# Kernel optimization log

Hardware: AMD Instinct MI355X
Metric: run time of the kernel (lower is better)

## Reference

```python
import jax, jax.numpy as jnp
from jax import lax
import numpy as np

B, N = 2, 1024  # batch of NxN linear-system matrices
DN = ('NCHW', 'OIHW', 'NCHW')


def _conv(x, w, b, pad):
    # cross-correlation, same convention as torch/spconv
    return lax.conv_general_dilated(x, w, (1, 1), pad, dimension_numbers=DN) + b[None, :, None, None]


def _spread_mask(m, pad):
    # regular sparse conv: output site active iff any input site in 2x2 window is active
    ones = jnp.ones((1, 1, 2, 2), dtype=m.dtype)
    return (lax.conv_general_dilated(m, ones, (1, 1), pad, dimension_numbers=DN) > 0).astype(m.dtype)


def _prelu(x, a):
    return jnp.where(x >= 0, x, a * x)


def setup_inputs() -> dict:
    key = jax.random.key(0)
    ks = jax.random.split(key, 10)
    mask = jax.random.randint(ks[0], (B, N, N), 0, 2, dtype=jnp.int32)
    x = jax.random.normal(ks[1], (B, 1, N, N), dtype=jnp.float32)

    def w(k, o, i, kh, kw):
        return jax.random.normal(k, (o, i, kh, kw), dtype=jnp.float32) / np.sqrt(i * kh * kw)

    def bias(k, o):
        return 0.01 * jax.random.normal(k, (o,), dtype=jnp.float32)

    return {
        'x': x, 'mask': mask,
        'w1': w(ks[2], 8, 1, 1, 1), 'b1': bias(ks[6], 8), 'a1': jnp.float32(0.25),
        'w2': w(ks[3], 16, 8, 2, 2), 'b2': bias(ks[7], 16), 'a2': jnp.float32(0.25),
        'w3': w(ks[4], 8, 16, 2, 2), 'b3': bias(ks[8], 8), 'a3': jnp.float32(0.25),
        'w4': w(ks[5], 1, 8, 1, 1), 'b4': bias(ks[9], 1),
    }


def reference(x, mask, w1, b1, a1, w2, b2, a2, w3, b3, a3, w4, b4):
    m = (mask > 0).astype(jnp.float32)[:, None]          # [B,1,N,N] active-site mask
    h = x * m                                            # sparse input: zeros at inactive sites
    # layer 1: 1x1 conv + PReLU (mask unchanged)
    h = _conv(h, w1, b1, ((0, 0), (0, 0))) * m
    h = _prelu(h, a1)
    # layer 2: 2x2 conv, padding (1,0) -> [B,16,N+1,N-1]
    p2 = ((1, 1), (0, 0))
    m2 = _spread_mask(m, p2)
    h = _conv(h, w2, b2, p2) * m2
    h = _prelu(h, a2)
    # layer 3: 2x2 conv, padding (0,1) -> [B,8,N,N]
    p3 = ((0, 0), (1, 1))
    m3 = _spread_mask(m2, p3)
    h = _conv(h, w3, b3, p3) * m3
    h = _prelu(h, a3)
    # layer 4: 1x1 conv (mask unchanged)
    h = _conv(h, w4, b4, ((0, 0), (0, 0))) * m3          # [B,1,N,N]
    # triangular masking on sparse indices (row=indices[:,1], col=indices[:,2])
    row = jnp.arange(N)[:, None]
    col = jnp.arange(N)[None, :]
    h = jnp.where((row >= col)[None, None], h, jnp.float32(0))
    diag_active = (row == col)[None, None] & (m3 > 0)
    h = jnp.where(diag_active, jax.nn.softplus(h), h)
    return h
```

## Files before the change

### kernel.cpp

```cpp
#include <hip/hip_runtime.h>
#include <hip/hip_bf16.h>
#include <math.h>

#define N 1024
#define TB 16

typedef __attribute__((ext_vector_type(8))) short short8;
typedef __attribute__((ext_vector_type(4))) short short4v;
typedef __attribute__((ext_vector_type(4))) float f32x4;

__device__ __forceinline__ float prelu(float v, float a) {
    return fmaxf(v, a * v);
}

__device__ __forceinline__ short f2bf(float f) {
    return (short)__bfloat16_as_ushort(__float2bfloat16(f));
}

__global__ __launch_bounds__(256, 8) void precond_mfma(
    const float* __restrict__ xg, const int* __restrict__ maskg,
    const float* __restrict__ w1, const float* __restrict__ b1, const float* __restrict__ a1p,
    const float* __restrict__ w2, const float* __restrict__ b2, const float* __restrict__ a2p,
    const float* __restrict__ w3, const float* __restrict__ b3, const float* __restrict__ a3p,
    const float* __restrict__ w4, const float* __restrict__ b4p,
    float* __restrict__ out)
{
    const int tid = threadIdx.x;
    const int bz  = blockIdx.z;
    const int t   = blockIdx.x;

    int by = (int)((sqrtf(8.0f * (float)t + 1.0f) - 1.0f) * 0.5f);
    by += ((by + 1) * (by + 2) / 2 <= t);
    by -= (by * (by + 1) / 2 > t);
    const int bx = t - by * (by + 1) / 2;
    const int ty0 = by * TB, tx0 = bx * TB;
    const bool diag = (bx == by);

    const int lane = tid & 63, wid = tid >> 6;
    const int c16 = lane & 15, g = lane >> 4;

    const float w2r0 = w2[tid];
    const float w2r1 = w2[tid + 256];
    const float w3r0 = w3[tid];
    const float w3r1 = w3[tid + 256];

    const int pA0 = tid;
    const int pA1 = tid + 256;
    const bool s1valid = (pA1 < 324);
    const bool s1wave  = ((tid - lane) + 256 < 324);
    const int dyA0 = pA0 / 18, dxA0 = pA0 - dyA0 * 18;
    const int dyA1 = pA1 / 18, dxA1 = pA1 - dyA1 * 18;

    int gy0 = ty0 - 1 + dyA0, gx0 = tx0 - 1 + dxA0;
    const bool in0 = (unsigned)gy0 < N && (unsigned)gx0 < N;
    size_t i0 = in0 ? (((size_t)bz * N + gy0) * N + gx0) : 0;
    const int   mr0 = maskg[i0];
    const float xr0 = xg[i0];

    int mr1 = 0; float xr1 = 0.f; bool in1 = false;
    if (s1wave) {
        int gy1 = ty0 - 1 + dyA1, gx1 = tx0 - 1 + dxA1;
        in1 = s1valid && (unsigned)gy1 < N && (unsigned)gx1 < N;
        size_t i1 = in1 ? (((size_t)bz * N + gy1) * N + gx1) : 0;
        mr1 = maskg[i1];
        xr1 = xg[i1];
    }

    if (by < 63 && tid < 64) {
        int zy = bx * TB + (tid >> 2), zx = (by + 1) * TB + (tid & 3) * 4;
        *(float4*)&out[((size_t)bz * N + zy) * N + zx] = make_float4(0.f, 0.f, 0.f, 0.f);
    }

    __shared__ __align__(16) short sW2[512];
    __shared__ __align__(16) short sW3h[512];
    __shared__ __align__(16) short h1s[324 * 8];
    __shared__ __align__(16) short h2lo[4][85 * 8];
    __shared__ __align__(16) short h2hi[4][85 * 8];
    __shared__ __align__(16) unsigned RM1[12];

    const float a1 = a1p[0], a2 = a2p[0], a3 = a3p[0];
    const float b4 = b4p[0];
    const bool leftEdge  = (tx0 == 0);
    const bool rightEdge = (tx0 == N - TB);

    {
        int s0 = tid, s1 = tid + 256;
        sW2[(s0 & ~31) | ((s0 & 3) << 3) | ((s0 >> 2) & 7)] = f2bf(w2r0);
        sW2[(s1 & ~31) | ((s1 & 3) << 3) | ((s1 >> 2) & 7)] = f2bf(w2r1);
        sW3h[(s0 & ~63) | ((s0 & 3) << 4) | ((s0 >> 2) & 15)] = f2bf(w3r0);
        sW3h[(s1 & ~63) | ((s1 & 3) << 4) | ((s1 >> 2) & 15)] = f2bf(w3r1);
    }

    {
        bool mb = in0 && (mr0 > 0);
        float xv = in0 ? xr0 : 0.f;
        unsigned long long bal = __ballot(mb);
        if (lane == 0) *(uint2*)&RM1[2 * wid] = make_uint2((unsigned)bal, (unsigned)(bal >> 32));
        short8 hv;
#pragma unroll
        for (int ch = 0; ch < 8; ++ch) hv[ch] = f2bf(prelu(fmaf(xv, w1[ch], b1[ch]), a1));
        if (!mb) hv = (short8)0;
        *(short8*)&h1s[pA0 * 8] = hv;

        if (s1wave) {
            bool mb1 = in1 && (mr1 > 0);
            float xv1 = in1 ? xr1 : 0.f;
            unsigned long long bal1 = __ballot(mb1);
            if (lane == 0) *(uint2*)&RM1[2 * (wid + 4)] = make_uint2((unsigned)bal1, (unsigned)(bal1 >> 32));
            if (s1valid) {
                short8 hv1;
#pragma unroll
                for (int ch = 0; ch < 8; ++ch) hv1[ch] = f2bf(prelu(fmaf(xv1, w1[ch], b1[ch]), a1));
                if (!mb1) hv1 = (short8)0;
                *(short8*)&h1s[pA1 * 8] = hv1;
            }
        }
    }
    __syncthreads();

    unsigned m2row[5];
    unsigned col16bits;
    {
        const int bitbase = 72 * wid;
        unsigned rr[6];
#pragma unroll
        for (int i = 0; i < 6; ++i) {
            int bit = bitbase + 18 * i;
            int w = bit >> 5, sh = bit & 31;
            unsigned long long v = ((unsigned long long)RM1[w + 1] << 32) | RM1[w];
            rr[i] = (unsigned)(v >> sh);
        }
#pragma unroll
        for (int i = 0; i < 5; ++i) {
            unsigned u = rr[i] | rr[i + 1];
            m2row[i] = (u | (u >> 1)) & 0x1FFFFu;
        }
        if (leftEdge) {
#pragma unroll
            for (int i = 0; i < 5; ++i) m2row[i] &= ~1u;
        }
        if (rightEdge) {
#pragma unroll
            for (int i = 0; i < 5; ++i) m2row[i] &= ~(1u << 16);
        }
        col16bits = ((m2row[0] >> 16) & 1u)        | (((m2row[1] >> 16) & 1u) << 1)
                  | (((m2row[2] >> 16) & 1u) << 2) | (((m2row[3] >> 16) & 1u) << 3)
                  | (((m2row[4] >> 16) & 1u) << 4);
    }

    {
        short8 a2f = *(const short8*)&sW2[c16 * 32 + g * 8];
        const int kh = g >> 1, kw = g & 1;
        const int rowbase = wid * 4;
        f32x4 bias2;
#pragma unroll
        for (int r = 0; r < 4; ++r) bias2[r] = b2[g * 4 + r];

        short* dst = (g & 2) ? &h2hi[wid][0] : &h2lo[wid][0];
        const int choff = (g & 1) * 4;

#pragma unroll
        for (int grp = 0; grp < 5; ++grp) {
            short8 bf = *(const short8*)&h1s[((rowbase + grp + kh) * 18 + c16 + kw) * 8];
            f32x4 acc = __builtin_amdgcn_mfma_f32_16x16x32_bf16(a2f, bf, bias2, 0, 0, 0);
            unsigned m2 = (m2row[grp] >> c16) & 1u;
            short4v hv;
#pragma unroll
            for (int r = 0; r < 4; ++r) hv[r] = f2bf(prelu(acc[r], a2));
            if (m2 == 0) { hv[0] = 0; hv[1] = 0; hv[2] = 0; hv[3] = 0; }
            *(short4v*)&dst[(grp * 17 + c16) * 8 + choff] = hv;
        }
        {
            int lrc = (c16 < 5) ? c16 : 4;
            short8 bf = *(const short8*)&h1s[((rowbase + lrc + kh) * 18 + 16 + kw) * 8];
            f32x4 acc = __builtin_amdgcn_mfma_f32_16x16x32_bf16(a2f, bf, bias2, 0, 0, 0);
            unsigned m2 = (col16bits >> c16) & 1u;
            short4v hv;
#pragma unroll
            for (int r = 0; r < 4; ++r) hv[r] = f2bf(prelu(acc[r], a2));
            if (m2 == 0) { hv[0] = 0; hv[1] = 0; hv[2] = 0; hv[3] = 0; }
            if (c16 < 5) *(short4v*)&dst[(lrc * 17 + 16) * 8 + choff] = hv;
        }
    }

    {
        short8 a3f0 = *(const short8*)&sW3h[(c16 & 7) * 64 + g * 8];
        short8 a3f1 = *(const short8*)&sW3h[(c16 & 7) * 64 + 32 + g * 8];
        if (c16 >= 8) { a3f0 = (short8)0; a3f1 = (short8)0; }
        const int kwC = g >> 1, ic8 = g & 1;
        const short* h2sel = ic8 ? &h2hi[wid][0] : &h2lo[wid][0];
        f32x4 bias3;
        float w4r[4];
#pragma unroll
        for (int r = 0; r < 4; ++r) {
            bias3[r] = (g < 2) ? b3[g * 4 + r] : 0.f;
            w4r[r]   = (g < 2) ? w4[g * 4 + r] : 0.f;
        }

        short8 bfp = *(const short8*)&h2sel[(c16 + kwC) * 8];
#pragma unroll
        for (int j = 0; j < 4; ++j) {
            short8 bfn = *(const short8*)&h2sel[((j + 1) * 17 + c16 + kwC) * 8];
            f32x4 acc = __builtin_amdgcn_mfma_f32_16x16x32_bf16(a3f0, bfp, bias3, 0, 0, 0);
            acc = __builtin_amdgcn_mfma_f32_16x16x32_bf16(a3f1, bfn, acc, 0, 0, 0);
            bfp = bfn;

            float partial = 0.f;
#pragma unroll
            for (int r = 0; r < 4; ++r) partial = fmaf(prelu(acc[r], a3), w4r[r], partial);
            partial += __shfl_xor(partial, 16, 64);

            if (g == 0) {
                unsigned combined = m2row[j] | m2row[j + 1];
                unsigned m3 = (combined >> c16) & 3u;
                float outv = m3 ? (partial + b4) : 0.f;
                int y = ty0 + wid * 4 + j, x = tx0 + c16;
                if (diag) {
                    if (y < x) {
                        outv = 0.f;
                    } else if (y == x && m3) {
                        outv = fmaxf(outv, 0.f) + log1pf(expf(-fabsf(outv)));
                    }
                }
                out[((size_t)bz * N + y) * N + x] = outv;
            }
        }
    }
}

extern "C" void kernel_launch(void* const* d_in, const int* in_sizes, int n_in,
                              void* d_out, int out_size, void* d_ws, size_t ws_size,
                              hipStream_t stream) {
    const float* x    = (const float*)d_in[0];
    const int*   mask = (const int*)  d_in[1];
    const float* w1   = (const float*)d_in[2];
    const float* b1   = (const float*)d_in[3];
    const float* a1   = (const float*)d_in[4];
    const float* w2   = (const float*)d_in[5];
    const float* b2   = (const float*)d_in[6];
    const float* a2   = (const float*)d_in[7];
    const float* w3   = (const float*)d_in[8];
    const float* b3   = (const float*)d_in[9];
    const float* a3   = (const float*)d_in[10];
    const float* w4   = (const float*)d_in[11];
    const float* b4   = (const float*)d_in[12];
    float* out = (float*)d_out;

    dim3 grid(2080, 1, 2);
    precond_mfma<<<grid, 256, 0, stream>>>(x, mask, w1, b1, a1, w2, b2, a2,
                                           w3, b3, a3, w4, b4, out);
}
```

Measured before the change: 24.38 us.

## Split each tile across eight waves of two rows with 512-thread blocks

Doubles the block to 512 threads so each of eight waves computes two output rows instead of four waves computing four. Every input halo site is then loaded by its own thread in a single pass, which removes the second conditional load and layer-1 pass. The cost is more recomputed layer-2 halo rows per wave (three rows for two outputs instead of five for four) and about 188 idle threads in the load stage. The launch-bounds hint is raised to match, which may tighten the register budget.

```diff
diff --git a/kernel.cpp b/kernel.cpp
--- a/kernel.cpp
+++ b/kernel.cpp
@@ -17,7 +17,7 @@
     return (short)__bfloat16_as_ushort(__float2bfloat16(f));
 }
 
-__global__ __launch_bounds__(256, 8) void precond_mfma(
+__global__ __launch_bounds__(512, 8) void precond_mfma(
     const float* __restrict__ xg, const int* __restrict__ maskg,
     const float* __restrict__ w1, const float* __restrict__ b1, const float* __restrict__ a1p,
     const float* __restrict__ w2, const float* __restrict__ b2, const float* __restrict__ a2p,
@@ -39,33 +39,17 @@
     const int lane = tid & 63, wid = tid >> 6;
     const int c16 = lane & 15, g = lane >> 4;
 
-    const float w2r0 = w2[tid];
-    const float w2r1 = w2[tid + 256];
-    const float w3r0 = w3[tid];
-    const float w3r1 = w3[tid + 256];
-
-    const int pA0 = tid;
-    const int pA1 = tid + 256;
-    const bool s1valid = (pA1 < 324);
-    const bool s1wave  = ((tid - lane) + 256 < 324);
-    const int dyA0 = pA0 / 18, dxA0 = pA0 - dyA0 * 18;
-    const int dyA1 = pA1 / 18, dxA1 = pA1 - dyA1 * 18;
-
-    int gy0 = ty0 - 1 + dyA0, gx0 = tx0 - 1 + dxA0;
-    const bool in0 = (unsigned)gy0 < N && (unsigned)gx0 < N;
+    const float w2r = w2[tid];
+    const float w3r = w3[tid];
+
+    const bool pvalid = (tid < 324);
+    const int dyA = tid / 18, dxA = tid - dyA * 18;
+    int gy0 = ty0 - 1 + dyA, gx0 = tx0 - 1 + dxA;
+    const bool in0 = pvalid && (unsigned)gy0 < N && (unsigned)gx0 < N;
     size_t i0 = in0 ? (((size_t)bz * N + gy0) * N + gx0) : 0;
     const int   mr0 = maskg[i0];
     const float xr0 = xg[i0];
 
-    int mr1 = 0; float xr1 = 0.f; bool in1 = false;
-    if (s1wave) {
-        int gy1 = ty0 - 1 + dyA1, gx1 = tx0 - 1 + dxA1;
-        in1 = s1valid && (unsigned)gy1 < N && (unsigned)gx1 < N;
-        size_t i1 = in1 ? (((size_t)bz * N + gy1) * N + gx1) : 0;
-        mr1 = maskg[i1];
-        xr1 = xg[i1];
-    }
-
     if (by < 63 && tid < 64) {
         int zy = bx * TB + (tid >> 2), zx = (by + 1) * TB + (tid & 3) * 4;
         *(float4*)&out[((size_t)bz * N + zy) * N + zx] = make_float4(0.f, 0.f, 0.f, 0.f);
@@ -74,84 +58,67 @@
     __shared__ __align__(16) short sW2[512];
     __shared__ __align__(16) short sW3h[512];
     __shared__ __align__(16) short h1s[324 * 8];
-    __shared__ __align__(16) short h2lo[4][85 * 8];
-    __shared__ __align__(16) short h2hi[4][85 * 8];
-    __shared__ __align__(16) unsigned RM1[12];
+    __shared__ __align__(16) short h2lo[8][51 * 8];
+    __shared__ __align__(16) short h2hi[8][51 * 8];
+    __shared__ __align__(16) unsigned RM1[16];
 
     const float a1 = a1p[0], a2 = a2p[0], a3 = a3p[0];
     const float b4 = b4p[0];
     const bool leftEdge  = (tx0 == 0);
     const bool rightEdge = (tx0 == N - TB);
 
-    {
-        int s0 = tid, s1 = tid + 256;
-        sW2[(s0 & ~31) | ((s0 & 3) << 3) | ((s0 >> 2) & 7)] = f2bf(w2r0);
-        sW2[(s1 & ~31) | ((s1 & 3) << 3) | ((s1 >> 2) & 7)] = f2bf(w2r1);
-        sW3h[(s0 & ~63) | ((s0 & 3) << 4) | ((s0 >> 2) & 15)] = f2bf(w3r0);
-        sW3h[(s1 & ~63) | ((s1 & 3) << 4) | ((s1 >> 2) & 15)] = f2bf(w3r1);
-    }
+    sW2[(tid & ~31) | ((tid & 3) << 3) | ((tid >> 2) & 7)] = f2bf(w2r);
+    sW3h[(tid & ~63) | ((tid & 3) << 4) | ((tid >> 2) & 15)] = f2bf(w3r);
 
     {
         bool mb = in0 && (mr0 > 0);
         float xv = in0 ? xr0 : 0.f;
         unsigned long long bal = __ballot(mb);
         if (lane == 0) *(uint2*)&RM1[2 * wid] = make_uint2((unsigned)bal, (unsigned)(bal >> 32));
-        short8 hv;
-#pragma unroll
-        for (int ch = 0; ch < 8; ++ch) hv[ch] = f2bf(prelu(fmaf(xv, w1[ch], b1[ch]), a1));
-        if (!mb) hv = (short8)0;
-        *(short8*)&h1s[pA0 * 8] = hv;
-
-        if (s1wave) {
-            bool mb1 = in1 && (mr1 > 0);
-            float xv1 = in1 ? xr1 : 0.f;
-            unsigned long long bal1 = __ballot(mb1);
-            if (lane == 0) *(uint2*)&RM1[2 * (wid + 4)] = make_uint2((unsigned)bal1, (unsigned)(bal1 >> 32));
-            if (s1valid) {
-                short8 hv1;
-#pragma unroll
-                for (int ch = 0; ch < 8; ++ch) hv1[ch] = f2bf(prelu(fmaf(xv1, w1[ch], b1[ch]), a1));
-                if (!mb1) hv1 = (short8)0;
-                *(short8*)&h1s[pA1 * 8] = hv1;
-            }
+        if (pvalid) {
+            short8 hv;
+#pragma unroll
+            for (int ch = 0; ch < 8; ++ch) hv[ch] = f2bf(prelu(fmaf(xv, w1[ch], b1[ch]), a1));
+            if (!mb) hv = (short8)0;
+            *(short8*)&h1s[tid * 8] = hv;
         }
     }
     __syncthreads();
 
-    unsigned m2row[5];
+    unsigned m2row[3];
     unsigned col16bits;
     {
-        const int bitbase = 72 * wid;
-        unsigned rr[6];
-#pragma unroll
-        for (int i = 0; i < 6; ++i) {
+        const int bitbase = 36 * wid;
+        unsigned rr[4];
+#pragma unroll
+        for (int i = 0; i < 4; ++i) {
             int bit = bitbase + 18 * i;
             int w = bit >> 5, sh = bit & 31;
             unsigned long long v = ((unsigned long long)RM1[w + 1] << 32) | RM1[w];
             rr[i] = (unsigned)(v >> sh);
         }
 #pragma unroll
-        for (int i = 0; i < 5; ++i) {
+        for (int i = 0; i < 3; ++i) {
             unsigned u = rr[i] | rr[i + 1];
             m2row[i] = (u | (u >> 1)) & 0x1FFFFu;
         }
         if (leftEdge) {
 #pragma unroll
-            for (int i = 0; i < 5; ++i) m2row[i] &= ~1u;
+            for (int i = 0; i < 3; ++i) m2row[i] &= ~1u;
         }
         if (rightEdge) {
 #pragma unroll
-            for (int i = 0; i < 5; ++i) m2row[i] &= ~(1u << 16);
-        }
-        col16bits = ((m2row[0] >> 16) & 1u)        | (((m2row[1] >> 16) & 1u) << 1)
-                  | (((m2row[2] >> 16) & 1u) << 2) | (((m2row[3] >> 16) & 1u) << 3)
-                  | (((m2row[4] >> 16) & 1u) << 4);
+            for (int i = 0; i < 3; ++i) m2row[i] &= ~(1u << 16);
+        }
+        col16bits = ((m2row[0] >> 16) & 1u)
+                  | (((m2row[1] >> 16) & 1u) << 1)
+                  | (((m2row[2] >> 16) & 1u) << 2);
     }
 
     {
         short8 a2f = *(const short8*)&sW2[c16 * 32 + g * 8];
         const int kh = g >> 1, kw = g & 1;
-        const int rowbase = wid * 4;
+        const int rowbase = wid * 2;
         f32x4 bias2;
 #pragma unroll
         for (int r = 0; r < 4; ++r) bias2[r] = b2[g * 4 + r];
@@ -160,7 +127,7 @@
         const int choff = (g & 1) * 4;
 
 #pragma unroll
-        for (int grp = 0; grp < 5; ++grp) {
+        for (int grp = 0; grp < 3; ++grp) {
             short8 bf = *(const short8*)&h1s[((rowbase + grp + kh) * 18 + c16 + kw) * 8];
             f32x4 acc = __builtin_amdgcn_mfma_f32_16x16x32_bf16(a2f, bf, bias2, 0, 0, 0);
             unsigned m2 = (m2row[grp] >> c16) & 1u;
@@ -171,7 +138,7 @@
             *(short4v*)&dst[(grp * 17 + c16) * 8 + choff] = hv;
         }
         {
-            int lrc = (c16 < 5) ? c16 : 4;
+            int lrc = (c16 < 3) ? c16 : 2;
             short8 bf = *(const short8*)&h1s[((rowbase + lrc + kh) * 18 + 16 + kw) * 8];
             f32x4 acc = __builtin_amdgcn_mfma_f32_16x16x32_bf16(a2f, bf, bias2, 0, 0, 0);
             unsigned m2 = (col16bits >> c16) & 1u;
@@ -179,7 +146,7 @@
 #pragma unroll
             for (int r = 0; r < 4; ++r) hv[r] = f2bf(prelu(acc[r], a2));
             if (m2 == 0) { hv[0] = 0; hv[1] = 0; hv[2] = 0; hv[3] = 0; }
-            if (c16 < 5) *(short4v*)&dst[(lrc * 17 + 16) * 8 + choff] = hv;
+            if (c16 < 3) *(short4v*)&dst[(lrc * 17 + 16) * 8 + choff] = hv;
         }
     }
 
@@ -199,7 +166,7 @@
 
         short8 bfp = *(const short8*)&h2sel[(c16 + kwC) * 8];
 #pragma unroll
-        for (int j = 0; j < 4; ++j) {
+        for (int j = 0; j < 2; ++j) {
             short8 bfn = *(const short8*)&h2sel[((j + 1) * 17 + c16 + kwC) * 8];
             f32x4 acc = __builtin_amdgcn_mfma_f32_16x16x32_bf16(a3f0, bfp, bias3, 0, 0, 0);
             acc = __builtin_amdgcn_mfma_f32_16x16x32_bf16(a3f1, bfn, acc, 0, 0, 0);
@@ -214,7 +181,7 @@
                 unsigned combined = m2row[j] | m2row[j + 1];
                 unsigned m3 = (combined >> c16) & 3u;
                 float outv = m3 ? (partial + b4) : 0.f;
-                int y = ty0 + wid * 4 + j, x = tx0 + c16;
+                int y = ty0 + wid * 2 + j, x = tx0 + c16;
                 if (diag) {
                     if (y < x) {
                         outv = 0.f;
@@ -247,6 +214,6 @@
     float* out = (float*)d_out;
 
     dim3 grid(2080, 1, 2);
-    precond_mfma<<<grid, 256, 0, stream>>>(x, mask, w1, b1, a1, w2, b2, a2,
+    precond_mfma<<<grid, 512, 0, stream>>>(x, mask, w1, b1, a1, w2, b2, a2,
                                            w3, b3, a3, w4, b4, out);
 }
```

New measurement: 26.59 us. +9.1%, slower.
